# Kernel optimization log

Measured on AMD Instinct MI355X. Metric: run time of the kernel, lower is better.

## Reference

```python
import jax, jax.numpy as jnp
import numpy as np

WEIGHT_FACTOR = 0.8


def _pairwise_l2(f):
    # ||a-b|| via GEMM trick: ||a||^2 + ||b||^2 - 2 a.b, avoiding the [N,N,D] blowup.
    sqn = jnp.sum(f * f, axis=1)                      # [N]
    sq = sqn[:, None] + sqn[None, :] - 2.0 * (f @ f.T)  # [N,N]
    sq = jnp.maximum(sq, 0.0)
    pos = sq > 0
    # safe sqrt: subgradient 0 at zero distance (matches torch.norm at 0)
    return jnp.where(pos, jnp.sqrt(jnp.where(pos, sq, 1.0)), 0.0)


def _mse(a, b):
    d = a - b
    return jnp.mean(d * d)


def setup_inputs() -> dict:
    key = jax.random.key(0)
    ks = jax.random.split(key, 8)
    N, D, C = 4096, 256, 1000
    return {
        "pred": jax.random.normal(ks[0], (N, C), dtype=jnp.float32),
        "target": jax.random.normal(ks[1], (N, C), dtype=jnp.float32),
        "pred_f0": jax.random.normal(ks[2], (N, D), dtype=jnp.float32),
        "pred_f1": jax.random.normal(ks[3], (N, D), dtype=jnp.float32),
        "pred_f2": jax.random.normal(ks[4], (N, D), dtype=jnp.float32),
        "target_f0": jax.random.normal(ks[5], (N, D), dtype=jnp.float32),
        "target_f1": jax.random.normal(ks[6], (N, D), dtype=jnp.float32),
        "target_f2": jax.random.normal(ks[7], (N, D), dtype=jnp.float32),
    }


def reference(pred, target, pred_f0, pred_f1, pred_f2, target_f0, target_f1, target_f2):
    pred_feats = (pred_f0, pred_f1, pred_f2)
    target_feats = (target_f0, target_f1, target_f2)
    num_features = len(pred_feats)

    label_loss = _mse(pred, target)
    feature_loss = 0.0
    for pf, tf in zip(pred_feats, target_feats):
        feature_loss = feature_loss + _mse(_pairwise_l2(pf), _pairwise_l2(tf))
    return (1.0 - WEIGHT_FACTOR) * label_loss + WEIGHT_FACTOR * feature_loss / num_features
```

## Files before the change

### kernel.cpp

```cpp
#include <hip/hip_runtime.h>
#include <stdint.h>

#define NR 4096
#define DD 256
#define NC_TOT 4096000
#define TILES 32
#define NTRI 528
#define NBLK_GRAM 512

typedef float f32x4 __attribute__((ext_vector_type(4)));
typedef unsigned char u8;

#define WS_MSEP_OFF  256
#define WS_FEATP_OFF 16384
#define WS_SQN_OFF   32768
#define WS_FP8_OFF   131072

__global__ __launch_bounds__(256) void prep_mse_kernel(
    const float* __restrict__ m0, const float* __restrict__ m1,
    const float* __restrict__ m2, const float* __restrict__ m3,
    const float* __restrict__ m4, const float* __restrict__ m5,
    u8* __restrict__ q8, float* __restrict__ sqn, unsigned* __restrict__ cnt)
{
    const int t = threadIdx.x, w = t >> 6, lane = t & 63;
    const int y = blockIdx.y;
    if (y == 0 && blockIdx.x == 0 && t == 0) *cnt = 0u;

    const float* mp = m0;
    if (y == 1) mp = m1;
    else if (y == 2) mp = m2;
    else if (y == 3) mp = m3;
    else if (y == 4) mp = m4;
    else if (y == 5) mp = m5;
    const int R = blockIdx.x * 4 + w;
    const int P = R >> 7, rr = R & 127;
    const float4* src = (const float4*)(mp + (size_t)R * DD);
    float4 v = src[lane];
    float ss = v.x * v.x + v.y * v.y + v.z * v.z + v.w * v.w;
    unsigned lo = __builtin_amdgcn_cvt_pk_fp8_f32(v.x, v.y, 0u, false);
    unsigned hi = __builtin_amdgcn_cvt_pk_fp8_f32(v.z, v.w, 0u, false);
    unsigned packed = (lo & 0xffffu) | (hi << 16);
    size_t idx = ((size_t)(y * 32 + P) << 15)
                 + (size_t)(lane >> 1) * 1024 + rr * 8 + (lane & 1) * 4;
    *(unsigned*)(q8 + idx) = packed;
    #pragma unroll
    for (int off = 32; off; off >>= 1) ss += __shfl_down(ss, off);
    if (lane == 0) sqn[(size_t)y * NR + R] = ss;
}

#define COMPUTE_DIRECT(PA, PB, ACC)                                            \
  do {                                                                         \
    _Pragma("unroll")                                                          \
    for (int kc = 0; kc < 8; kc++) {                                           \
      long a_[4], b_[2];                                                       \
      _Pragma("unroll")                                                        \
      for (int mi = 0; mi < 4; mi++)                                           \
        a_[mi] = *(const long*)((PA) + kc * 4096 + aoff + mi * 128);           \
      _Pragma("unroll")                                                        \
      for (int ni = 0; ni < 2; ni++)                                           \
        b_[ni] = *(const long*)((PB) + kc * 4096 + boff + ni * 128);           \
      _Pragma("unroll")                                                        \
      for (int mi = 0; mi < 4; mi++)                                           \
        _Pragma("unroll")                                                      \
        for (int ni = 0; ni < 2; ni++)                                         \
          ACC[mi][ni] = __builtin_amdgcn_mfma_f32_16x16x32_fp8_fp8(            \
              a_[mi], b_[ni], ACC[mi][ni], 0, 0, 0);                           \
    }                                                                          \
  } while (0)

#define RESET_ACC()                                                            \
  do {                                                                         \
    _Pragma("unroll")                                                          \
    for (int a4 = 0; a4 < 4; a4++)                                             \
      _Pragma("unroll")                                                        \
      for (int b2 = 0; b2 < 2; b2++) {                                         \
        accp[a4][b2] = f32x4{0.f, 0.f, 0.f, 0.f};                              \
        acct[a4][b2] = f32x4{0.f, 0.f, 0.f, 0.f};                              \
      }                                                                        \
  } while (0)

__global__ __launch_bounds__(512, 4) void gram_loss_kernel(
    const u8* __restrict__ q8, const float* __restrict__ sqn,
    const float4* __restrict__ pred, const float4* __restrict__ target,
    float* __restrict__ featp, float* __restrict__ msep,
    unsigned* __restrict__ cnt, float* __restrict__ out)
{
    __shared__ float s_red[8], s_mse[8];
    __shared__ int s_last;

    const int xcd = blockIdx.x & 7, slot = blockIdx.x >> 3;
    const int t = threadIdx.x;
    const int w = t >> 6, lane = t & 63;
    const int wm = w >> 2, wn = w & 3;
    const int quad = lane >> 4, l16 = lane & 15;
    const char* qb = (const char*)q8;

    const int aoff = quad * 1024 + (wm * 64 + l16) * 8;
    const int boff = quad * 1024 + (wn * 32 + l16) * 8;

    float mse = 0.f;
    for (int i = blockIdx.x * 512 + t; i < NC_TOT / 4; i += NBLK_GRAM * 512) {
        float4 x = pred[i], yv = target[i];
        float dx = x.x - yv.x, dy = x.y - yv.y;
        float dz = x.z - yv.z, dw = x.w - yv.w;
        mse += dx * dx + dy * dy + dz * dz + dw * dw;
    }

    auto tile_of = [&](int k, int& f, int& ti, int& tj) -> bool {
        int rs = (slot + k * 21 + xcd * 9) & 63;
        int idx = rs + (k << 6), lin;
        if (xcd < 6) {
            if (idx >= 196) return false;
            f = xcd >> 1; lin = (xcd & 1) + 2 * idx;
        } else {
            if (idx >= 204) return false;
            int rr = (xcd - 6) + 2 * idx;
            f = rr / 136; lin = 392 + rr - f * 136;
        }
        int a = 0, rem = lin;
        while (rem >= TILES - a) { rem -= TILES - a; a++; }
        ti = a; tj = a + rem;
        return true;
    };

    f32x4 accp[4][2], acct[4][2];
    RESET_ACC();

    float local = 0.f;

    int fc, tic, tjc;
    int k = 0;
    bool more = tile_of(0, fc, tic, tjc);
    while (more) {
        const char* pA = qb + (((size_t)(fc * 32 + tic)) << 15);
        const char* pB = qb + (((size_t)(fc * 32 + tjc)) << 15);
        const char* tA = qb + (((size_t)((3 + fc) * 32 + tic)) << 15);
        const char* tB = qb + (((size_t)((3 + fc) * 32 + tjc)) << 15);

        COMPUTE_DIRECT(pA, pB, accp);
        COMPUTE_DIRECT(tA, tB, acct);

        {
            const float* sqp = sqn + (size_t)fc * NR;
            const float* sqt = sqn + (size_t)(3 + fc) * NR;
            const bool diag = (tic == tjc);
            float tl = 0.f;
            #pragma unroll
            for (int mi = 0; mi < 4; mi++) {
                const int i0 = wm * 64 + mi * 16 + quad * 4;
                const f32x4 sip = *(const f32x4*)(sqp + tic * 128 + i0);
                const f32x4 sit = *(const f32x4*)(sqt + tic * 128 + i0);
                #pragma unroll
                for (int ni = 0; ni < 2; ni++) {
                    const int j_loc = wn * 32 + ni * 16 + l16;
                    const float spj = sqp[tjc * 128 + j_loc];
                    const float stj = sqt[tjc * 128 + j_loc];
                    const f32x4 gp = accp[mi][ni], gt = acct[mi][ni];
                    #pragma unroll
                    for (int r = 0; r < 4; r++) {
                        float dp2 = fmaxf(fmaf(-2.f, gp[r], sip[r] + spj), 0.f);
                        float dt2 = fmaxf(fmaf(-2.f, gt[r], sit[r] + stj), 0.f);
                        if (diag && (i0 + r == j_loc)) { dp2 = 0.f; dt2 = 0.f; }
                        float sq = __builtin_amdgcn_sqrtf(dp2 * dt2);
                        tl += fmaf(-2.f, sq, dp2 + dt2);
                    }
                }
            }
            local += diag ? tl : 2.f * tl;
            RESET_ACC();
        }
        k++;
        more = tile_of(k, fc, tic, tjc);
    }

    #pragma unroll
    for (int off = 32; off; off >>= 1) {
        local += __shfl_down(local, off);
        mse   += __shfl_down(mse, off);
    }
    if (lane == 0) { s_red[w] = local; s_mse[w] = mse; }
    __syncthreads();
    if (t == 0) {
        float bs = 0.f, ms = 0.f;
        #pragma unroll
        for (int i = 0; i < 8; i++) { bs += s_red[i]; ms += s_mse[i]; }
        featp[blockIdx.x] = bs;
        msep[blockIdx.x]  = ms;
        __threadfence();
        unsigned old = atomicAdd(cnt, 1u);
        s_last = (old == NBLK_GRAM - 1) ? 1 : 0;
    }
    __syncthreads();

    if (s_last) {
        __threadfence();
        float s2 = 0.f, m2 = 0.f;
        for (int i = t; i < NBLK_GRAM; i += 512) {
            s2 += featp[i];
            m2 += msep[i];
        }
        #pragma unroll
        for (int off = 32; off; off >>= 1) {
            s2 += __shfl_down(s2, off);
            m2 += __shfl_down(m2, off);
        }
        __shared__ float fr[8], mr[8];
        if (lane == 0) { fr[w] = s2; mr[w] = m2; }
        __syncthreads();
        if (t == 0) {
            float fs = 0.f, ms = 0.f;
            #pragma unroll
            for (int i = 0; i < 8; i++) { fs += fr[i]; ms += mr[i]; }
            out[0] = 0.2f * (ms / (float)NC_TOT) +
                     (0.8f / 3.0f) * (fs / ((float)NR * (float)NR));
        }
    }
}

extern "C" void kernel_launch(void* const* d_in, const int* in_sizes, int n_in,
                              void* d_out, int out_size, void* d_ws, size_t ws_size,
                              hipStream_t stream) {
    unsigned* cnt  = (unsigned*)d_ws;
    float* msep    = (float*)((char*)d_ws + WS_MSEP_OFF);
    float* featp   = (float*)((char*)d_ws + WS_FEATP_OFF);
    float* sqn     = (float*)((char*)d_ws + WS_SQN_OFF);
    u8* q8         = (u8*)((char*)d_ws + WS_FP8_OFF);

    prep_mse_kernel<<<dim3(1024, 6), 256, 0, stream>>>(
        (const float*)d_in[2], (const float*)d_in[3], (const float*)d_in[4],
        (const float*)d_in[5], (const float*)d_in[6], (const float*)d_in[7],
        q8, sqn, cnt);

    gram_loss_kernel<<<NBLK_GRAM, 512, 0, stream>>>(
        q8, sqn, (const float4*)d_in[0], (const float4*)d_in[1],
        featp, msep, cnt, (float*)d_out);
}
```

Baseline: 156.8 us.

## Stage A tiles into LDS via async global_load_lds and prefetch next tile

The A-operand tiles (pred and target) are now copied into a 64 KB shared buffer using direct global-to-LDS loads. The next tile is prefetched during the epilogue of the current one, while B still streams from global memory. MFMA sections are wrapped in s_setprio, and the first k-chunk starts from a zero accumulator instead of an explicit reset. This aims to cut redundant global loads of A across waves and hide load latency, at the cost of 64 KB of LDS per block, which will lower occupancy versus the requested 4 blocks per CU, and two extra barriers per tile.

```diff
diff --git a/kernel.cpp b/kernel.cpp
--- a/kernel.cpp
+++ b/kernel.cpp
@@ -48,17 +48,34 @@
     if (lane == 0) sqn[(size_t)y * NR + R] = ss;
 }
 
-#define COMPUTE_DIRECT(PA, PB, ACC)                                            \
+#define COMPUTE_HYB(ABASE, PB, ACC)                                            \
   do {                                                                         \
+    __builtin_amdgcn_s_setprio(1);                                             \
+    {                                                       \
+      long a_[4], b_[2];                                                       \
+      _Pragma("unroll")                                                        \
+      for (int mi = 0; mi < 4; mi++)                                           \
+        a_[mi] = *(const long*)&abuf[(ABASE) + quad * 1024 + aoff + mi * 128]; \
+      _Pragma("unroll")                                                        \
+      for (int ni = 0; ni < 2; ni++)                                           \
+        b_[ni] = *(const long*)((PB) + quad * 1024 + boff + ni * 128);         \
+      _Pragma("unroll")                                                        \
+      for (int mi = 0; mi < 4; mi++)                                           \
+        _Pragma("unroll")                                                      \
+        for (int ni = 0; ni < 2; ni++)                                         \
+          ACC[mi][ni] = __builtin_amdgcn_mfma_f32_16x16x32_fp8_fp8(            \
+              a_[mi], b_[ni], f32x4{0.f, 0.f, 0.f, 0.f}, 0, 0, 0);             \
+    }                                                                          \
     _Pragma("unroll")                                                          \
-    for (int kc = 0; kc < 8; kc++) {                                           \
+    for (int kc = 1; kc < 8; kc++) {                                           \
+      const int gg = kc * 4 + quad;                                            \
       long a_[4], b_[2];                                                       \
       _Pragma("unroll")                                                        \
       for (int mi = 0; mi < 4; mi++)                                           \
-        a_[mi] = *(const long*)((PA) + kc * 4096 + aoff + mi * 128);           \
+        a_[mi] = *(const long*)&abuf[(ABASE) + gg * 1024 + aoff + mi * 128];   \
       _Pragma("unroll")                                                        \
       for (int ni = 0; ni < 2; ni++)                                           \
-        b_[ni] = *(const long*)((PB) + kc * 4096 + boff + ni * 128);           \
+        b_[ni] = *(const long*)((PB) + gg * 1024 + boff + ni * 128);           \
       _Pragma("unroll")                                                        \
       for (int mi = 0; mi < 4; mi++)                                           \
         _Pragma("unroll")                                                      \
@@ -66,17 +83,7 @@
           ACC[mi][ni] = __builtin_amdgcn_mfma_f32_16x16x32_fp8_fp8(            \
               a_[mi], b_[ni], ACC[mi][ni], 0, 0, 0);                           \
     }                                                                          \
-  } while (0)
-
-#define RESET_ACC()                                                            \
-  do {                                                                         \
-    _Pragma("unroll")                                                          \
-    for (int a4 = 0; a4 < 4; a4++)                                             \
-      _Pragma("unroll")                                                        \
-      for (int b2 = 0; b2 < 2; b2++) {                                         \
-        accp[a4][b2] = f32x4{0.f, 0.f, 0.f, 0.f};                              \
-        acct[a4][b2] = f32x4{0.f, 0.f, 0.f, 0.f};                              \
-      }                                                                        \
+    __builtin_amdgcn_s_setprio(0);                                             \
   } while (0)
 
 __global__ __launch_bounds__(512, 4) void gram_loss_kernel(
@@ -85,6 +92,7 @@
     float* __restrict__ featp, float* __restrict__ msep,
     unsigned* __restrict__ cnt, float* __restrict__ out)
 {
+    __shared__ u8 abuf[65536];
     __shared__ float s_red[8], s_mse[8];
     __shared__ int s_last;
 
@@ -95,8 +103,8 @@
     const int quad = lane >> 4, l16 = lane & 15;
     const char* qb = (const char*)q8;
 
-    const int aoff = quad * 1024 + (wm * 64 + l16) * 8;
-    const int boff = quad * 1024 + (wn * 32 + l16) * 8;
+    const int aoff = (wm * 64 + l16) * 8;
+    const int boff = (wn * 32 + l16) * 8;
 
     float mse = 0.f;
     for (int i = blockIdx.x * 512 + t; i < NC_TOT / 4; i += NBLK_GRAM * 512) {
@@ -123,22 +131,38 @@
         return true;
     };
 
+    auto stage = [&](int f, int ti) {
+        const size_t bP = ((size_t)(f * 32 + ti)) << 15;
+        const size_t bT = ((size_t)((3 + f) * 32 + ti)) << 15;
+        const char* g = qb + ((w < 4) ? bP : bT) + (w & 3) * 8192 + lane * 16;
+        char* l = (char*)abuf + ((w < 4) ? 0 : 32768) + (w & 3) * 8192;
+        #pragma unroll
+        for (int i = 0; i < 8; i++)
+            __builtin_amdgcn_global_load_lds(
+                (const __attribute__((address_space(1))) void*)(g + i * 1024),
+                (__attribute__((address_space(3))) void*)(l + i * 1024), 16, 0, 0);
+    };
+
     f32x4 accp[4][2], acct[4][2];
-    RESET_ACC();
-
     float local = 0.f;
 
     int fc, tic, tjc;
+    tile_of(0, fc, tic, tjc);
+    stage(fc, tic);
+
     int k = 0;
-    bool more = tile_of(0, fc, tic, tjc);
-    while (more) {
-        const char* pA = qb + (((size_t)(fc * 32 + tic)) << 15);
+    while (true) {
+        __syncthreads();
+
         const char* pB = qb + (((size_t)(fc * 32 + tjc)) << 15);
-        const char* tA = qb + (((size_t)((3 + fc) * 32 + tic)) << 15);
         const char* tB = qb + (((size_t)((3 + fc) * 32 + tjc)) << 15);
-
-        COMPUTE_DIRECT(pA, pB, accp);
-        COMPUTE_DIRECT(tA, tB, acct);
+        COMPUTE_HYB(0,     pB, accp);
+        COMPUTE_HYB(32768, tB, acct);
+
+        int fn, tin, tjn;
+        const bool more = tile_of(k + 1, fn, tin, tjn);
+        __syncthreads();
+        if (more) stage(fn, tin);
 
         {
             const float* sqp = sqn + (size_t)fc * NR;
@@ -167,10 +191,10 @@
                 }
             }
             local += diag ? tl : 2.f * tl;
-            RESET_ACC();
-        }
+        }
+        if (!more) break;
         k++;
-        more = tile_of(k, fc, tic, tjc);
+        fc = fn; tic = tin; tjc = tjn;
     }
 
     #pragma unroll
```

Result: faster. 145.4 us (-7.3%).

## Stage fp8 tiles through LDS with double-buffered async loads and 32x32x64 scaled MFMA

Applied to the files above, without the earlier changes.

Changes the fp8 quantized layout to row-major 256-byte rows and stages each K-half of the A/B tiles into a double-buffered LDS area using global_load_lds, prefetching the next stage while the current one computes. The 16x16x32 fp8 MFMAs read directly from global memory are replaced by the 32x32x64 scaled f8f6f4 MFMA with unit scales, and the epilogue is remapped to the 32x32 accumulator layout. This aims to remove global-load latency stalls and reduce MFMA instruction count, at the cost of 64KB of LDS per block, several barriers per tile, and possible occupancy loss.

```diff
diff --git a/kernel.cpp b/kernel.cpp
--- a/kernel.cpp
+++ b/kernel.cpp
@@ -9,12 +9,17 @@
 #define NBLK_GRAM 512
 
 typedef float f32x4 __attribute__((ext_vector_type(4)));
+typedef float f32x16 __attribute__((ext_vector_type(16)));
+typedef int   i32x4 __attribute__((ext_vector_type(4)));
+typedef int   i32x8 __attribute__((ext_vector_type(8)));
 typedef unsigned char u8;
 
 #define WS_MSEP_OFF  256
 #define WS_FEATP_OFF 16384
 #define WS_SQN_OFF   32768
 #define WS_FP8_OFF   131072
+
+#define SCALE1 0x7F7F7F7F
 
 __global__ __launch_bounds__(256) void prep_mse_kernel(
     const float* __restrict__ m0, const float* __restrict__ m1,
@@ -40,43 +45,42 @@
     unsigned lo = __builtin_amdgcn_cvt_pk_fp8_f32(v.x, v.y, 0u, false);
     unsigned hi = __builtin_amdgcn_cvt_pk_fp8_f32(v.z, v.w, 0u, false);
     unsigned packed = (lo & 0xffffu) | (hi << 16);
-    size_t idx = ((size_t)(y * 32 + P) << 15)
-                 + (size_t)(lane >> 1) * 1024 + rr * 8 + (lane & 1) * 4;
+    size_t idx = ((size_t)(y * 32 + P) << 15) + (size_t)rr * 256 + lane * 4;
     *(unsigned*)(q8 + idx) = packed;
     #pragma unroll
     for (int off = 32; off; off >>= 1) ss += __shfl_down(ss, off);
     if (lane == 0) sqn[(size_t)y * NR + R] = ss;
 }
 
-#define COMPUTE_DIRECT(PA, PB, ACC)                                            \
+#define COMPUTE_STAGE(BI, ACC, ZC)                                             \
   do {                                                                         \
+    const u8* tA_ = &buf[BI][0];                                               \
+    const u8* tB_ = &buf[BI][16384];                                           \
+    __builtin_amdgcn_s_setprio(1);                                             \
     _Pragma("unroll")                                                          \
-    for (int kc = 0; kc < 8; kc++) {                                           \
-      long a_[4], b_[2];                                                       \
+    for (int kc = 0; kc < 2; kc++) {                                           \
+      const int sb = (kc * 2 + q2) * 4096;                                     \
+      i32x4 bl = *(const i32x4*)&tB_[sb + boff];                               \
+      i32x4 bh = *(const i32x4*)&tB_[sb + 2048 + boff];                        \
+      i32x8 b_ = __builtin_shufflevector(bl, bh, 0, 1, 2, 3, 4, 5, 6, 7);      \
       _Pragma("unroll")                                                        \
-      for (int mi = 0; mi < 4; mi++)                                           \
-        a_[mi] = *(const long*)((PA) + kc * 4096 + aoff + mi * 128);           \
-      _Pragma("unroll")                                                        \
-      for (int ni = 0; ni < 2; ni++)                                           \
-        b_[ni] = *(const long*)((PB) + kc * 4096 + boff + ni * 128);           \
-      _Pragma("unroll")                                                        \
-      for (int mi = 0; mi < 4; mi++)                                           \
-        _Pragma("unroll")                                                      \
-        for (int ni = 0; ni < 2; ni++)                                         \
-          ACC[mi][ni] = __builtin_amdgcn_mfma_f32_16x16x32_fp8_fp8(            \
-              a_[mi], b_[ni], ACC[mi][ni], 0, 0, 0);                           \
+      for (int mi = 0; mi < 2; mi++) {                                         \
+        i32x4 al = *(const i32x4*)&tA_[sb + aoff + mi * 512];                   \
+        i32x4 ah = *(const i32x4*)&tA_[sb + 2048 + aoff + mi * 512];            \
+        i32x8 a_ = __builtin_shufflevector(al, ah, 0, 1, 2, 3, 4, 5, 6, 7);    \
+        if ((ZC) && kc == 0) {                                                 \
+          f32x16 z_;                                                           \
+          _Pragma("unroll")                                                    \
+          for (int j = 0; j < 16; j++) z_[j] = 0.f;                            \
+          ACC[mi] = __builtin_amdgcn_mfma_scale_f32_32x32x64_f8f6f4(           \
+              a_, b_, z_, 0, 0, 0, SCALE1, 0, SCALE1);                         \
+        } else {                                                               \
+          ACC[mi] = __builtin_amdgcn_mfma_scale_f32_32x32x64_f8f6f4(           \
+              a_, b_, ACC[mi], 0, 0, 0, SCALE1, 0, SCALE1);                    \
+        }                                                                      \
+      }                                                                        \
     }                                                                          \
-  } while (0)
-
-#define RESET_ACC()                                                            \
-  do {                                                                         \
-    _Pragma("unroll")                                                          \
-    for (int a4 = 0; a4 < 4; a4++)                                             \
-      _Pragma("unroll")                                                        \
-      for (int b2 = 0; b2 < 2; b2++) {                                         \
-        accp[a4][b2] = f32x4{0.f, 0.f, 0.f, 0.f};                              \
-        acct[a4][b2] = f32x4{0.f, 0.f, 0.f, 0.f};                              \
-      }                                                                        \
+    __builtin_amdgcn_s_setprio(0);                                             \
   } while (0)
 
 __global__ __launch_bounds__(512, 4) void gram_loss_kernel(
@@ -85,6 +89,7 @@
     float* __restrict__ featp, float* __restrict__ msep,
     unsigned* __restrict__ cnt, float* __restrict__ out)
 {
+    __shared__ __align__(16) u8 buf[2][32768];
     __shared__ float s_red[8], s_mse[8];
     __shared__ int s_last;
 
@@ -92,11 +97,11 @@
     const int t = threadIdx.x;
     const int w = t >> 6, lane = t & 63;
     const int wm = w >> 2, wn = w & 3;
-    const int quad = lane >> 4, l16 = lane & 15;
+    const int q2 = lane >> 5, l31 = lane & 31;
     const char* qb = (const char*)q8;
 
-    const int aoff = quad * 1024 + (wm * 64 + l16) * 8;
-    const int boff = quad * 1024 + (wn * 32 + l16) * 8;
+    const int aoff = (wm * 64 + l31) * 16;
+    const int boff = (wn * 32 + l31) * 16;
 
     float mse = 0.f;
     for (int i = blockIdx.x * 512 + t; i < NC_TOT / 4; i += NBLK_GRAM * 512) {
@@ -123,54 +128,88 @@
         return true;
     };
 
-    f32x4 accp[4][2], acct[4][2];
-    RESET_ACC();
-
+    auto prefetch = [&](int b, int m, int ti, int tj, int kk) {
+        const size_t bA = ((size_t)(m * 32 + ti)) << 15;
+        const size_t bB = ((size_t)(m * 32 + tj)) << 15;
+        const int w4 = w & 3;
+        const char* g = qb + ((w < 4) ? bA : bB)
+                        + (size_t)lane * 256 + kk * 128 + w4 * 32;
+        char* l = (char*)&buf[b][0] + ((w < 4) ? 0 : 16384) + w4 * 4096
+                  + lane * 16;
+        __builtin_amdgcn_global_load_lds(
+            (const __attribute__((address_space(1))) void*)(g),
+            (__attribute__((address_space(3))) void*)(l), 16, 0, 0);
+        __builtin_amdgcn_global_load_lds(
+            (const __attribute__((address_space(1))) void*)(g + 16384),
+            (__attribute__((address_space(3))) void*)(l + 1024), 16, 0, 0);
+        __builtin_amdgcn_global_load_lds(
+            (const __attribute__((address_space(1))) void*)(g + 16),
+            (__attribute__((address_space(3))) void*)(l + 2048), 16, 0, 0);
+        __builtin_amdgcn_global_load_lds(
+            (const __attribute__((address_space(1))) void*)(g + 16400),
+            (__attribute__((address_space(3))) void*)(l + 3072), 16, 0, 0);
+    };
+
+    f32x16 accp[2], acct[2];
     float local = 0.f;
 
     int fc, tic, tjc;
+    tile_of(0, fc, tic, tjc);
+    prefetch(0, fc, tic, tjc, 0);
+    __syncthreads();
+
     int k = 0;
-    bool more = tile_of(0, fc, tic, tjc);
-    while (more) {
-        const char* pA = qb + (((size_t)(fc * 32 + tic)) << 15);
-        const char* pB = qb + (((size_t)(fc * 32 + tjc)) << 15);
-        const char* tA = qb + (((size_t)((3 + fc) * 32 + tic)) << 15);
-        const char* tB = qb + (((size_t)((3 + fc) * 32 + tjc)) << 15);
-
-        COMPUTE_DIRECT(pA, pB, accp);
-        COMPUTE_DIRECT(tA, tB, acct);
+    while (true) {
+        prefetch(1, fc, tic, tjc, 1);
+        COMPUTE_STAGE(0, accp, 1);
+        __syncthreads();
+
+        prefetch(0, 3 + fc, tic, tjc, 0);
+        COMPUTE_STAGE(1, accp, 0);
+        __syncthreads();
+
+        prefetch(1, 3 + fc, tic, tjc, 1);
+        COMPUTE_STAGE(0, acct, 1);
+        __syncthreads();
+
+        int fn, tin, tjn;
+        const bool more = tile_of(k + 1, fn, tin, tjn);
+        if (more) prefetch(0, fn, tin, tjn, 0);
+        COMPUTE_STAGE(1, acct, 0);
 
         {
             const float* sqp = sqn + (size_t)fc * NR;
             const float* sqt = sqn + (size_t)(3 + fc) * NR;
             const bool diag = (tic == tjc);
+            const int jg = wn * 32 + l31;
+            const float spj = sqp[tjc * 128 + jg];
+            const float stj = sqt[tjc * 128 + jg];
             float tl = 0.f;
             #pragma unroll
-            for (int mi = 0; mi < 4; mi++) {
-                const int i0 = wm * 64 + mi * 16 + quad * 4;
-                const f32x4 sip = *(const f32x4*)(sqp + tic * 128 + i0);
-                const f32x4 sit = *(const f32x4*)(sqt + tic * 128 + i0);
+            for (int mi = 0; mi < 2; mi++) {
                 #pragma unroll
-                for (int ni = 0; ni < 2; ni++) {
-                    const int j_loc = wn * 32 + ni * 16 + l16;
-                    const float spj = sqp[tjc * 128 + j_loc];
-                    const float stj = sqt[tjc * 128 + j_loc];
-                    const f32x4 gp = accp[mi][ni], gt = acct[mi][ni];
+                for (int g4 = 0; g4 < 4; g4++) {
+                    const int i0 = wm * 64 + mi * 32 + g4 * 8 + q2 * 4;
+                    const f32x4 sip = *(const f32x4*)(sqp + tic * 128 + i0);
+                    const f32x4 sit = *(const f32x4*)(sqt + tic * 128 + i0);
                     #pragma unroll
-                    for (int r = 0; r < 4; r++) {
-                        float dp2 = fmaxf(fmaf(-2.f, gp[r], sip[r] + spj), 0.f);
-                        float dt2 = fmaxf(fmaf(-2.f, gt[r], sit[r] + stj), 0.f);
-                        if (diag && (i0 + r == j_loc)) { dp2 = 0.f; dt2 = 0.f; }
+                    for (int r4 = 0; r4 < 4; r4++) {
+                        const int r = g4 * 4 + r4;
+                        float gp = accp[mi][r], gt = acct[mi][r];
+                        float dp2 = fmaxf(fmaf(-2.f, gp, sip[r4] + spj), 0.f);
+                        float dt2 = fmaxf(fmaf(-2.f, gt, sit[r4] + stj), 0.f);
+                        if (diag && (i0 + r4 == jg)) { dp2 = 0.f; dt2 = 0.f; }
                         float sq = __builtin_amdgcn_sqrtf(dp2 * dt2);
                         tl += fmaf(-2.f, sq, dp2 + dt2);
                     }
                 }
             }
             local += diag ? tl : 2.f * tl;
-            RESET_ACC();
-        }
+        }
+        __syncthreads();
+        if (!more) break;
         k++;
-        more = tile_of(k, fc, tic, tjc);
+        fc = fn; tic = tin; tjc = tjn;
     }
 
     #pragma unroll
```

Measured after the change: 192.0 us. 1.22x slower.
